# Performance work log

Measured on AMD Instinct MI355X. Metric: run time of the kernel, lower is better.

The kernel has to match this reference:

```python
import jax, jax.numpy as jnp
import numpy as np

B, Nres, TOP_K, NUM_RBF = 2, 2048, 30, 16
MAX_REL = 32  # positional clip range -> 2*32+2 = 66 classes


def _gather_nodes(nodes, idx):
    # nodes: [B, N, ...], idx: [B, N, K] -> [B, N, K, ...]
    return jax.vmap(lambda n, i: n[i])(nodes, idx)


def _rbf(D):
    # D: [..., ] -> [..., NUM_RBF]; mu in [2, 22], sigma = 20/16
    mu = jnp.linspace(2.0, 22.0, NUM_RBF)
    sigma = (22.0 - 2.0) / NUM_RBF
    return jnp.exp(-(((D[..., None] - mu) / sigma) ** 2))


def setup_inputs() -> dict:
    key = jax.random.key(0)
    ks = jax.random.split(key, 4)
    X = jax.random.normal(ks[0], (B, Nres, 4, 3), dtype=jnp.float32) * 3.0
    mask = jnp.ones((B, Nres), dtype=jnp.float32)
    residue_idx = jnp.broadcast_to(jnp.arange(Nres, dtype=jnp.int32)[None], (B, Nres))
    chain_labels = jnp.zeros((B, Nres), dtype=jnp.int32)
    w_pos = jax.random.normal(ks[1], (66, 16), dtype=jnp.float32) * 0.05
    b_pos = jax.random.normal(ks[2], (16,), dtype=jnp.float32) * 0.05
    w_edge = jax.random.normal(ks[3], (416, 128), dtype=jnp.float32) * 0.05
    ln_gamma = jnp.ones((128,), dtype=jnp.float32)
    ln_beta = jnp.zeros((128,), dtype=jnp.float32)
    return dict(X=X, mask=mask, residue_idx=residue_idx, chain_labels=chain_labels,
                w_pos=w_pos, b_pos=b_pos, w_edge=w_edge, ln_gamma=ln_gamma, ln_beta=ln_beta)


def reference(X, mask, residue_idx, chain_labels, w_pos, b_pos, w_edge, ln_gamma, ln_beta):
    # virtual C-beta from N, C, Ca (atom order in X: N=0, C=1, Ca=2, O=3)
    b = X[:, :, 2, :] - X[:, :, 0, :]
    c = X[:, :, 1, :] - X[:, :, 2, :]
    a = jnp.cross(b, c)
    Cb = -0.58273431 * a + 0.56802827 * b - 0.54067466 * c + X[:, :, 2, :]
    N_, C, Ca, O = X[:, :, 0, :], X[:, :, 1, :], X[:, :, 2, :], X[:, :, 3, :]

    # masked kNN on C atoms (ProteinFeatures._dist)
    m2 = mask[:, None, :] * mask[:, :, None]                       # [B,N,N]
    dX = C[:, None, :, :] - C[:, :, None, :]
    D = m2 * jnp.sqrt(jnp.sum(dX ** 2, -1) + 1e-6)
    D_max = jnp.max(D, -1, keepdims=True)
    D_adj = D + (1.0 - m2) * D_max
    neg, E_idx = jax.lax.top_k(-D_adj, TOP_K)                      # smallest-k
    D_neighbors = -neg                                             # [B,N,K]

    # 25-channel RBF features; gather neighbor coords instead of NxN per pair
    atoms = jnp.stack([N_, Ca, Cb, C, O], 0)                       # [5,B,N,3]
    gathered = jax.vmap(lambda A: _gather_nodes(A, E_idx))(atoms)  # [5,B,N,K,3]
    # pair order follows torch source: NN,CaCa,CbCb,CN,CCa,CCb,NCa,NCb,CbCa,
    # NC,CaC,CbC,CaN,CbN,CaCb,OO,CO,OC,NO,ON,CbO,OCa,OCb,CaO  (0=N,1=Ca,2=Cb,3=C,4=O)
    pa = jnp.array([0, 1, 2, 3, 3, 3, 0, 0, 2, 0, 1, 2, 1, 2, 1, 4, 3, 4, 0, 4, 2, 4, 4, 1])
    pb = jnp.array([0, 1, 2, 0, 1, 2, 1, 2, 1, 3, 3, 3, 0, 0, 2, 4, 4, 3, 4, 0, 4, 1, 2, 4])
    A_sel = atoms[pa]                                              # [24,B,N,3]
    Bn_sel = gathered[pb]                                          # [24,B,N,K,3]
    Dp = jnp.sqrt(jnp.sum((A_sel[:, :, :, None, :] - Bn_sel) ** 2, -1) + 1e-6)
    RBF_all = jnp.concatenate([_rbf(D_neighbors)[None], _rbf(Dp)], 0)  # [25,B,N,K,16]
    RBF_all = jnp.moveaxis(RBF_all, 0, 3).reshape(B, Nres, TOP_K, 25 * NUM_RBF)

    # positional encodings over gathered offsets / chain match
    offset = residue_idx[:, :, None] - _gather_nodes(residue_idx, E_idx)   # [B,N,K]
    E_chains = (chain_labels[:, :, None] == _gather_nodes(chain_labels, E_idx)).astype(jnp.int32)
    d = jnp.clip(offset + MAX_REL, 0, 2 * MAX_REL) * E_chains + (1 - E_chains) * (2 * MAX_REL + 1)
    E_pos = w_pos[d] + b_pos                                       # one_hot @ W == gather

    # edge embedding + layernorm
    E = jnp.concatenate([E_pos, RBF_all], -1) @ w_edge             # [B,N,K,128]
    mu = E.mean(-1, keepdims=True)
    var = E.var(-1, keepdims=True)
    E = (E - mu) / jnp.sqrt(var + 1e-5) * ln_gamma + ln_beta
    return E, E_idx
```

## Files before the change

kernel.cpp:

```cpp
#include <hip/hip_runtime.h>
#include <hip/hip_bf16.h>
#include <stdint.h>

#define BB    2
#define NRES  2048
#define TOPK  30
#define NRBF  16
#define NFEAT 416
#define NCH   128
#define NS8   108
#define NKT   13

typedef __attribute__((ext_vector_type(4))) float f32x4;
typedef unsigned long long u64;

__constant__ int c_pa[24] = {0,1,2,3,3,3,0,0,2,0,1,2,1,2,1,4,3,4,0,4,2,4,4,1};
__constant__ int c_pb[24] = {0,1,2,0,1,2,1,2,1,3,3,3,0,0,2,4,4,3,4,0,4,1,2,4};

static __device__ __forceinline__ unsigned pack4_fp8(float f0, float f1, float f2, float f3) {
  unsigned r = 0;
  r = __builtin_amdgcn_cvt_pk_fp8_f32(f0, f1, r, false);
  r = __builtin_amdgcn_cvt_pk_fp8_f32(f2, f3, r, true);
  return r;
}

__global__ __launch_bounds__(256) void prep_kernel(const float* __restrict__ X,
                                                   const float* __restrict__ w_edge,
                                                   float* __restrict__ atoms,
                                                   float4* __restrict__ Cpk,
                                                   unsigned* __restrict__ wB8) {
  if (blockIdx.x < 16) {
    int id = blockIdx.x * 256 + threadIdx.x;
    const float* x = X + (size_t)id * 12;
    float nx = x[0], ny = x[1], nz = x[2];
    float cx = x[3], cy = x[4], cz = x[5];
    float ax = x[6], ay = x[7], az = x[8];
    float ox = x[9], oy = x[10], oz = x[11];
    float bx = ax - nx, by = ay - ny, bz = az - nz;
    float ccx = cx - ax, ccy = cy - ay, ccz = cz - az;
    float crx = by * ccz - bz * ccy;
    float cry = bz * ccx - bx * ccz;
    float crz = bx * ccy - by * ccx;
    float cbx = -0.58273431f * crx + 0.56802827f * bx - 0.54067466f * ccx + ax;
    float cby = -0.58273431f * cry + 0.56802827f * by - 0.54067466f * ccy + ay;
    float cbz = -0.58273431f * crz + 0.56802827f * bz - 0.54067466f * ccz + az;
    float* r = atoms + (size_t)id * 16;
    r[0] = nx;  r[1] = ny;  r[2] = nz;
    r[3] = ax;  r[4] = ay;  r[5] = az;
    r[6] = cbx; r[7] = cby; r[8] = cbz;
    r[9] = cx;  r[10] = cy; r[11] = cz;
    r[12] = ox; r[13] = oy; r[14] = oz;
    r[15] = 0.f;
    Cpk[id] = make_float4(cx, cy, cz, 0.f);
  } else {
    int id = (blockIdx.x - 16) * 256 + threadIdx.x;
    if (id >= NFEAT * NCH / 4) return;
    int bb   = id * 4;
    int j0   = bb & 7;
    int lane = (bb >> 3) & 63;
    int nt   = (bb >> 9) & 7;
    int kt   = bb >> 12;
    int col  = nt * 16 + (lane & 15);
    int kb   = kt * 32 + ((lane >> 4) << 3) + j0;
    float f0 = w_edge[(size_t)(kb + 0) * NCH + col];
    float f1 = w_edge[(size_t)(kb + 1) * NCH + col];
    float f2 = w_edge[(size_t)(kb + 2) * NCH + col];
    float f3 = w_edge[(size_t)(kb + 3) * NCH + col];
    wB8[id] = pack4_fp8(f0, f1, f2, f3);
  }
}

__global__ __launch_bounds__(256) void topk_kernel(const float4* __restrict__ Cpk,
                                                   int* __restrict__ eidx,
                                                   float* __restrict__ dn,
                                                   float* __restrict__ outI) {
  int tid = threadIdx.x;
  int lane = tid & 63;
  int bi = blockIdx.x * 4 + (tid >> 6);
  int b = bi >> 11;
  int i = bi & (NRES - 1);
  const float4* Cb = Cpk + (size_t)b * NRES;
  float4 ci = Cb[i];

  u64 key[4][8];
  u64 sub[4];
#pragma unroll
  for (int g = 0; g < 4; ++g) {
    sub[g] = ~0ull;
#pragma unroll
    for (int s = 0; s < 8; ++s) {
      int j = lane + 64 * (g * 8 + s);
      float4 cj = Cb[j];
      float dx = cj.x - ci.x, dy = cj.y - ci.y, dz = cj.z - ci.z;
      float sm = __fadd_rn(__fadd_rn(__fadd_rn(__fmul_rn(dx, dx), __fmul_rn(dy, dy)),
                                     __fmul_rn(dz, dz)), 1e-6f);
      float d = sqrtf(sm);
      key[g][s] = ((u64)__float_as_uint(d) << 32) | (unsigned)j;
      if (key[g][s] < sub[g]) sub[g] = key[g][s];
    }
  }

  for (int k = 0; k < TOPK; ++k) {
    u64 m01 = sub[0] < sub[1] ? sub[0] : sub[1];
    u64 m23 = sub[2] < sub[3] ? sub[2] : sub[3];
    u64 gm = m01 < m23 ? m01 : m23;
#pragma unroll
    for (int off = 32; off; off >>= 1) {
      u64 o = __shfl_xor(gm, off, 64);
      if (o < gm) gm = o;
    }
    if (lane == 0) {
      int idx = (int)(unsigned)(gm & 0xffffffffu);
      eidx[(size_t)bi * TOPK + k] = idx;
      dn[(size_t)bi * TOPK + k] = __uint_as_float((unsigned)(gm >> 32));
      outI[(size_t)bi * TOPK + k] = (float)idx;
    }
#pragma unroll
    for (int g = 0; g < 4; ++g) {
      if (sub[g] == gm) {
        sub[g] = ~0ull;
#pragma unroll
        for (int s = 0; s < 8; ++s) {
          if (key[g][s] == gm) key[g][s] = ~0ull;
          if (key[g][s] < sub[g]) sub[g] = key[g][s];
        }
      }
    }
  }
}

__global__ __launch_bounds__(256) void edge_mfma_kernel(
    const float* __restrict__ atoms, const int* __restrict__ eidx_g,
    const float* __restrict__ dn_g, const int* __restrict__ ridx,
    const int* __restrict__ chain, const float* __restrict__ w_pos,
    const float* __restrict__ b_pos, const unsigned* __restrict__ wB8,
    const float* __restrict__ gamma, const float* __restrict__ beta,
    float* __restrict__ outE) {
  __shared__ __align__(16) unsigned feat8[32 * NS8];
  __shared__ float nat[TOPK][16];
  __shared__ float iat[16];
  __shared__ float dn_s[TOPK];
  __shared__ int   dsel[TOPK];
  __shared__ float2 lnp[32][4];

  int tid = threadIdx.x;
  int bi = blockIdx.x;
  int b = bi >> 11;
  int nq = tid >> 6, lane = tid & 63;
  int q = lane >> 4, ccol = lane & 15;

  if (tid < TOPK) {
    dn_s[tid] = dn_g[(size_t)bi * TOPK + tid];
    int j = eidx_g[(size_t)bi * TOPK + tid];
    int off = ridx[bi] - ridx[b * NRES + j];
    int ec = (chain[bi] == chain[b * NRES + j]) ? 1 : 0;
    int d = off + 32; d = d < 0 ? 0 : (d > 64 ? 64 : d);
    dsel[tid] = ec ? d : 65;
  }
  if (tid >= 64 && tid < 80) iat[tid - 64] = atoms[(size_t)bi * 16 + (tid - 64)];
  for (int idx = tid; idx < TOPK * 16; idx += 256) {
    int e = idx >> 4, f = idx & 15;
    nat[e][f] = atoms[((size_t)(b * NRES) + eidx_g[(size_t)bi * TOPK + e]) * 16 + f];
  }
  for (int idx = tid; idx < 2 * NS8; idx += 256)
    feat8[30 * NS8 + idx] = 0u;
  __syncthreads();

  if (tid < TOPK * 4) {
    int e = tid >> 2, p = tid & 3;
    int f0 = p * 4, ds = dsel[e];
    feat8[e * NS8 + p] = pack4_fp8(w_pos[ds * 16 + f0 + 0] + b_pos[f0 + 0],
                                   w_pos[ds * 16 + f0 + 1] + b_pos[f0 + 1],
                                   w_pos[ds * 16 + f0 + 2] + b_pos[f0 + 2],
                                   w_pos[ds * 16 + f0 + 3] + b_pos[f0 + 3]);
  }
  for (int idx = tid; idx < TOPK * 25; idx += 256) {
    int e = idx / 25, g = idx - e * 25;
    float d;
    if (g == 0) {
      d = dn_s[e];
    } else {
      int qq = g - 1;
      const float* A  = &iat[c_pa[qq] * 3];
      const float* Bv = &nat[e][c_pb[qq] * 3];
      float dx = A[0] - Bv[0], dy = A[1] - Bv[1], dz = A[2] - Bv[2];
      d = sqrtf(dx * dx + dy * dy + dz * dz + 1e-6f);
    }
    float v[16];
#pragma unroll
    for (int j = 0; j < 16; ++j) {
      float mu = 2.0f + (float)j * (20.0f / 15.0f);
      float t = (d - mu) * 0.8f;
      v[j] = __expf(-t * t);
    }
    uint4 w4 = make_uint4(pack4_fp8(v[0], v[1], v[2], v[3]),
                          pack4_fp8(v[4], v[5], v[6], v[7]),
                          pack4_fp8(v[8], v[9], v[10], v[11]),
                          pack4_fp8(v[12], v[13], v[14], v[15]));
    *(uint4*)&feat8[e * NS8 + 4 + 4 * g] = w4;
  }
  __syncthreads();

  const unsigned* ar0 = &feat8[ccol * NS8];
  const unsigned* ar1 = &feat8[(16 + ccol) * NS8];
  const u64* wBll = (const u64*)wB8;

  f32x4 acc00 = {}, acc01 = {}, acc10 = {}, acc11 = {};
#pragma unroll
  for (int kt = 0; kt < NKT; ++kt) {
    union { unsigned u[2]; long long l; } a0, a1;
    int ao = kt * 8 + q * 2;
    a0.u[0] = ar0[ao]; a0.u[1] = ar0[ao + 1];
    a1.u[0] = ar1[ao]; a1.u[1] = ar1[ao + 1];
    long long b0 = (long long)wBll[(size_t)(kt * 8 + nq * 2 + 0) * 64 + lane];
    long long b1 = (long long)wBll[(size_t)(kt * 8 + nq * 2 + 1) * 64 + lane];
    acc00 = __builtin_amdgcn_mfma_f32_16x16x32_fp8_fp8(a0.l, b0, acc00, 0, 0, 0);
    acc01 = __builtin_amdgcn_mfma_f32_16x16x32_fp8_fp8(a0.l, b1, acc01, 0, 0, 0);
    acc10 = __builtin_amdgcn_mfma_f32_16x16x32_fp8_fp8(a1.l, b0, acc10, 0, 0, 0);
    acc11 = __builtin_amdgcn_mfma_f32_16x16x32_fp8_fp8(a1.l, b1, acc11, 0, 0, 0);
  }

#pragma unroll
  for (int mh = 0; mh < 2; ++mh) {
#pragma unroll
    for (int reg = 0; reg < 4; ++reg) {
      float v0 = mh ? acc10[reg] : acc00[reg];
      float v1 = mh ? acc11[reg] : acc01[reg];
      float s = v0 + v1, ss = v0 * v0 + v1 * v1;
      s  += __shfl_xor(s, 1, 64);  ss += __shfl_xor(ss, 1, 64);
      s  += __shfl_xor(s, 2, 64);  ss += __shfl_xor(ss, 2, 64);
      s  += __shfl_xor(s, 4, 64);  ss += __shfl_xor(ss, 4, 64);
      s  += __shfl_xor(s, 8, 64);  ss += __shfl_xor(ss, 8, 64);
      if (ccol == 0) lnp[(mh << 4) + q * 4 + reg][nq] = make_float2(s, ss);
    }
  }
  __syncthreads();

  float g0 = gamma[(nq * 2 + 0) * 16 + ccol], be0 = beta[(nq * 2 + 0) * 16 + ccol];
  float g1 = gamma[(nq * 2 + 1) * 16 + ccol], be1 = beta[(nq * 2 + 1) * 16 + ccol];
#pragma unroll
  for (int mh = 0; mh < 2; ++mh) {
#pragma unroll
    for (int reg = 0; reg < 4; ++reg) {
      int m = (mh << 4) + q * 4 + reg;
      if (m < TOPK) {
        float2 p0 = lnp[m][0], p1 = lnp[m][1], p2 = lnp[m][2], p3 = lnp[m][3];
        float s = (p0.x + p1.x) + (p2.x + p3.x);
        float ss = (p0.y + p1.y) + (p2.y + p3.y);
        float mu = s * (1.0f / 128.0f);
        float var = ss * (1.0f / 128.0f) - mu * mu;
        float rstd = rsqrtf(var + 1e-5f);
        float va = mh ? acc10[reg] : acc00[reg];
        float vb = mh ? acc11[reg] : acc01[reg];
        float* o = outE + ((size_t)bi * TOPK + m) * NCH + ccol;
        o[(nq * 2 + 0) * 16] = (va - mu) * rstd * g0 + be0;
        o[(nq * 2 + 1) * 16] = (vb - mu) * rstd * g1 + be1;
      }
    }
  }
}

extern "C" void kernel_launch(void* const* d_in, const int* in_sizes, int n_in,
                              void* d_out, int out_size, void* d_ws, size_t ws_size,
                              hipStream_t stream) {
  const float* X      = (const float*)d_in[0];
  const int*   ridx   = (const int*)d_in[2];
  const int*   chain  = (const int*)d_in[3];
  const float* w_pos  = (const float*)d_in[4];
  const float* b_pos  = (const float*)d_in[5];
  const float* w_edge = (const float*)d_in[6];
  const float* gamma  = (const float*)d_in[7];
  const float* beta   = (const float*)d_in[8];

  float* outE = (float*)d_out;
  float* outI = outE + (size_t)BB * NRES * TOPK * NCH;

  char* p = (char*)d_ws;
  float* atoms = (float*)p;                 p += (size_t)BB * NRES * 16 * 4;
  int*   eidx  = (int*)p;                   p += (size_t)BB * NRES * TOPK * 4;
  float* dn    = (float*)p;                 p += (size_t)BB * NRES * TOPK * 4;
  unsigned* wB8 = (unsigned*)p;             p += (size_t)NCH * NFEAT;
  float4* Cpk  = (float4*)p;

  prep_kernel<<<16 + (NFEAT * NCH / 4 + 255) / 256, 256, 0, stream>>>(X, w_edge, atoms, Cpk, wB8);
  topk_kernel<<<BB * NRES / 4, 256, 0, stream>>>(Cpk, eidx, dn, outI);
  edge_mfma_kernel<<<BB * NRES, 256, 0, stream>>>(atoms, eidx, dn, ridx, chain,
                                                  w_pos, b_pos, wB8, gamma, beta, outE);
}
```

Measured before the change: 77.38 us.

## Extract two minima per top-k round and process two residues per edge block

The top-k kernel now tracks the two smallest keys per group and merges top-2 pairs across the wavefront, so each round emits two neighbors. This halves the number of shuffle-reduction rounds at the cost of more compare work per round. The edge MFMA kernel now handles two residues per block, reusing each loaded weight fragment across twice as many MFMAs and halving the block count. The price is more LDS per block and more accumulator registers, which may lower occupancy.

New measurement: 93.81 us. 1.21x slower.

```diff
diff --git a/kernel.cpp b/kernel.cpp
--- a/kernel.cpp
+++ b/kernel.cpp
@@ -10,6 +10,7 @@
 #define NCH   128
 #define NS8   108
 #define NKT   13
+#define RPB   2
 
 typedef __attribute__((ext_vector_type(4))) float f32x4;
 typedef unsigned long long u64;
@@ -23,6 +24,8 @@
   r = __builtin_amdgcn_cvt_pk_fp8_f32(f2, f3, r, true);
   return r;
 }
+static __device__ __forceinline__ u64 umin64(u64 a, u64 b) { return a < b ? a : b; }
+static __device__ __forceinline__ u64 umax64(u64 a, u64 b) { return a > b ? a : b; }
 
 __global__ __launch_bounds__(256) void prep_kernel(const float* __restrict__ X,
                                                    const float* __restrict__ w_edge,
@@ -62,11 +65,10 @@
     int kt   = bb >> 12;
     int col  = nt * 16 + (lane & 15);
     int kb   = kt * 32 + ((lane >> 4) << 3) + j0;
-    float f0 = w_edge[(size_t)(kb + 0) * NCH + col];
-    float f1 = w_edge[(size_t)(kb + 1) * NCH + col];
-    float f2 = w_edge[(size_t)(kb + 2) * NCH + col];
-    float f3 = w_edge[(size_t)(kb + 3) * NCH + col];
-    wB8[id] = pack4_fp8(f0, f1, f2, f3);
+    wB8[id] = pack4_fp8(w_edge[(size_t)(kb + 0) * NCH + col],
+                        w_edge[(size_t)(kb + 1) * NCH + col],
+                        w_edge[(size_t)(kb + 2) * NCH + col],
+                        w_edge[(size_t)(kb + 3) * NCH + col]);
   }
 }
 
@@ -83,10 +85,10 @@
   float4 ci = Cb[i];
 
   u64 key[4][8];
-  u64 sub[4];
+  u64 g1[4], g2[4];
 #pragma unroll
   for (int g = 0; g < 4; ++g) {
-    sub[g] = ~0ull;
+    g1[g] = ~0ull; g2[g] = ~0ull;
 #pragma unroll
     for (int s = 0; s < 8; ++s) {
       int j = lane + 64 * (g * 8 + s);
@@ -95,35 +97,49 @@
       float sm = __fadd_rn(__fadd_rn(__fadd_rn(__fmul_rn(dx, dx), __fmul_rn(dy, dy)),
                                      __fmul_rn(dz, dz)), 1e-6f);
       float d = sqrtf(sm);
-      key[g][s] = ((u64)__float_as_uint(d) << 32) | (unsigned)j;
-      if (key[g][s] < sub[g]) sub[g] = key[g][s];
-    }
-  }
-
-  for (int k = 0; k < TOPK; ++k) {
-    u64 m01 = sub[0] < sub[1] ? sub[0] : sub[1];
-    u64 m23 = sub[2] < sub[3] ? sub[2] : sub[3];
-    u64 gm = m01 < m23 ? m01 : m23;
+      u64 kk = ((u64)__float_as_uint(d) << 32) | (unsigned)j;
+      key[g][s] = kk;
+      if (kk < g1[g]) { g2[g] = g1[g]; g1[g] = kk; }
+      else if (kk < g2[g]) g2[g] = kk;
+    }
+  }
+
+  for (int kk2 = 0; kk2 < TOPK / 2; ++kk2) {
+    u64 x1 = umin64(g1[0], g1[1]);
+    u64 x2 = umin64(umax64(g1[0], g1[1]), umin64(g2[0], g2[1]));
+    u64 y1 = umin64(g1[2], g1[3]);
+    u64 y2 = umin64(umax64(g1[2], g1[3]), umin64(g2[2], g2[3]));
+    u64 m1 = umin64(x1, y1);
+    u64 m2 = umin64(umax64(x1, y1), umin64(x2, y2));
 #pragma unroll
     for (int off = 32; off; off >>= 1) {
-      u64 o = __shfl_xor(gm, off, 64);
-      if (o < gm) gm = o;
+      u64 o1 = __shfl_xor(m1, off, 64);
+      u64 o2 = __shfl_xor(m2, off, 64);
+      u64 n1 = umin64(m1, o1);
+      u64 n2 = umin64(umax64(m1, o1), umin64(m2, o2));
+      m1 = n1; m2 = n2;
     }
     if (lane == 0) {
-      int idx = (int)(unsigned)(gm & 0xffffffffu);
-      eidx[(size_t)bi * TOPK + k] = idx;
-      dn[(size_t)bi * TOPK + k] = __uint_as_float((unsigned)(gm >> 32));
-      outI[(size_t)bi * TOPK + k] = (float)idx;
+      int i1 = (int)(unsigned)m1, i2 = (int)(unsigned)m2;
+      size_t o = (size_t)bi * TOPK + 2 * kk2;
+      eidx[o] = i1;           eidx[o + 1] = i2;
+      dn[o]   = __uint_as_float((unsigned)(m1 >> 32));
+      dn[o+1] = __uint_as_float((unsigned)(m2 >> 32));
+      outI[o] = (float)i1;    outI[o + 1] = (float)i2;
     }
 #pragma unroll
     for (int g = 0; g < 4; ++g) {
-      if (sub[g] == gm) {
-        sub[g] = ~0ull;
+      bool hit = (g1[g] == m1) | (g1[g] == m2) | (g2[g] == m2);
+      if (hit) {
+        u64 n1 = ~0ull, n2 = ~0ull;
 #pragma unroll
         for (int s = 0; s < 8; ++s) {
-          if (key[g][s] == gm) key[g][s] = ~0ull;
-          if (key[g][s] < sub[g]) sub[g] = key[g][s];
+          u64 kv = key[g][s];
+          if (kv == m1 || kv == m2) { kv = ~0ull; key[g][s] = kv; }
+          if (kv < n1) { n2 = n1; n1 = kv; }
+          else if (kv < n2) n2 = kv;
         }
+        g1[g] = n1; g2[g] = n2;
       }
     }
   }
@@ -136,52 +152,62 @@
     const float* __restrict__ b_pos, const unsigned* __restrict__ wB8,
     const float* __restrict__ gamma, const float* __restrict__ beta,
     float* __restrict__ outE) {
-  __shared__ __align__(16) unsigned feat8[32 * NS8];
-  __shared__ float nat[TOPK][16];
-  __shared__ float iat[16];
-  __shared__ float dn_s[TOPK];
-  __shared__ int   dsel[TOPK];
-  __shared__ float2 lnp[32][4];
+  __shared__ __align__(16) unsigned feat8[RPB * 32 * NS8];
+  __shared__ float nat[RPB * TOPK][16];
+  __shared__ float iat[RPB][16];
+  __shared__ float dn_s[RPB * TOPK];
+  __shared__ int   dsel[RPB * TOPK];
+  __shared__ float2 lnp[RPB][32][4];
 
   int tid = threadIdx.x;
-  int bi = blockIdx.x;
-  int b = bi >> 11;
+  int bi0 = blockIdx.x * RPB;
+  int b = bi0 >> 11;
   int nq = tid >> 6, lane = tid & 63;
   int q = lane >> 4, ccol = lane & 15;
 
-  if (tid < TOPK) {
-    dn_s[tid] = dn_g[(size_t)bi * TOPK + tid];
-    int j = eidx_g[(size_t)bi * TOPK + tid];
-    int off = ridx[bi] - ridx[b * NRES + j];
-    int ec = (chain[bi] == chain[b * NRES + j]) ? 1 : 0;
+  if (tid < RPB * TOPK) {
+    int gi = bi0 + tid / TOPK;
+    int k = tid % TOPK;
+    dn_s[tid] = dn_g[(size_t)gi * TOPK + k];
+    int j = eidx_g[(size_t)gi * TOPK + k];
+    int off = ridx[gi] - ridx[b * NRES + j];
+    int ec = (chain[gi] == chain[b * NRES + j]) ? 1 : 0;
     int d = off + 32; d = d < 0 ? 0 : (d > 64 ? 64 : d);
     dsel[tid] = ec ? d : 65;
   }
-  if (tid >= 64 && tid < 80) iat[tid - 64] = atoms[(size_t)bi * 16 + (tid - 64)];
-  for (int idx = tid; idx < TOPK * 16; idx += 256) {
+  if (tid >= 64 && tid < 64 + RPB * 16) {
+    int t = tid - 64;
+    iat[t >> 4][t & 15] = atoms[((size_t)bi0 + (t >> 4)) * 16 + (t & 15)];
+  }
+  for (int idx = tid; idx < RPB * TOPK * 16; idx += 256) {
     int e = idx >> 4, f = idx & 15;
-    nat[e][f] = atoms[((size_t)(b * NRES) + eidx_g[(size_t)bi * TOPK + e]) * 16 + f];
-  }
-  for (int idx = tid; idx < 2 * NS8; idx += 256)
-    feat8[30 * NS8 + idx] = 0u;
+    int gi = bi0 + e / TOPK;
+    nat[e][f] = atoms[((size_t)(b * NRES) + eidx_g[(size_t)gi * TOPK + (e % TOPK)]) * 16 + f];
+  }
+  for (int idx = tid; idx < RPB * 2 * NS8; idx += 256) {
+    int r = idx / (2 * NS8), rem = idx % (2 * NS8);
+    feat8[(r * 32 + 30) * NS8 + rem] = 0u;
+  }
   __syncthreads();
 
-  if (tid < TOPK * 4) {
+  if (tid < RPB * TOPK * 4) {
     int e = tid >> 2, p = tid & 3;
     int f0 = p * 4, ds = dsel[e];
-    feat8[e * NS8 + p] = pack4_fp8(w_pos[ds * 16 + f0 + 0] + b_pos[f0 + 0],
-                                   w_pos[ds * 16 + f0 + 1] + b_pos[f0 + 1],
-                                   w_pos[ds * 16 + f0 + 2] + b_pos[f0 + 2],
-                                   w_pos[ds * 16 + f0 + 3] + b_pos[f0 + 3]);
-  }
-  for (int idx = tid; idx < TOPK * 25; idx += 256) {
+    int r = e / TOPK, k = e % TOPK;
+    feat8[(r * 32 + k) * NS8 + p] = pack4_fp8(w_pos[ds * 16 + f0 + 0] + b_pos[f0 + 0],
+                                              w_pos[ds * 16 + f0 + 1] + b_pos[f0 + 1],
+                                              w_pos[ds * 16 + f0 + 2] + b_pos[f0 + 2],
+                                              w_pos[ds * 16 + f0 + 3] + b_pos[f0 + 3]);
+  }
+  for (int idx = tid; idx < RPB * TOPK * 25; idx += 256) {
     int e = idx / 25, g = idx - e * 25;
+    int r = e / TOPK, k = e - r * TOPK;
     float d;
     if (g == 0) {
       d = dn_s[e];
     } else {
       int qq = g - 1;
-      const float* A  = &iat[c_pa[qq] * 3];
+      const float* A  = &iat[r][c_pa[qq] * 3];
       const float* Bv = &nat[e][c_pb[qq] * 3];
       float dx = A[0] - Bv[0], dy = A[1] - Bv[1], dz = A[2] - Bv[2];
       d = sqrtf(dx * dx + dy * dy + dz * dz + 1e-6f);
@@ -197,41 +223,54 @@
                           pack4_fp8(v[4], v[5], v[6], v[7]),
                           pack4_fp8(v[8], v[9], v[10], v[11]),
                           pack4_fp8(v[12], v[13], v[14], v[15]));
-    *(uint4*)&feat8[e * NS8 + 4 + 4 * g] = w4;
+    *(uint4*)&feat8[(r * 32 + k) * NS8 + 4 + 4 * g] = w4;
   }
   __syncthreads();
 
-  const unsigned* ar0 = &feat8[ccol * NS8];
-  const unsigned* ar1 = &feat8[(16 + ccol) * NS8];
+  const unsigned* ar00 = &feat8[(0 * 32 + ccol) * NS8];
+  const unsigned* ar01 = &feat8[(0 * 32 + 16 + ccol) * NS8];
+  const unsigned* ar10 = &feat8[(1 * 32 + ccol) * NS8];
+  const unsigned* ar11 = &feat8[(1 * 32 + 16 + ccol) * NS8];
   const u64* wBll = (const u64*)wB8;
 
-  f32x4 acc00 = {}, acc01 = {}, acc10 = {}, acc11 = {};
+  f32x4 a000 = {}, a001 = {}, a010 = {}, a011 = {};
+  f32x4 a100 = {}, a101 = {}, a110 = {}, a111 = {};
 #pragma unroll
   for (int kt = 0; kt < NKT; ++kt) {
-    union { unsigned u[2]; long long l; } a0, a1;
+    union { unsigned u[2]; long long l; } f00, f01, f10, f11;
     int ao = kt * 8 + q * 2;
-    a0.u[0] = ar0[ao]; a0.u[1] = ar0[ao + 1];
-    a1.u[0] = ar1[ao]; a1.u[1] = ar1[ao + 1];
+    f00.u[0] = ar00[ao]; f00.u[1] = ar00[ao + 1];
+    f01.u[0] = ar01[ao]; f01.u[1] = ar01[ao + 1];
+    f10.u[0] = ar10[ao]; f10.u[1] = ar10[ao + 1];
+    f11.u[0] = ar11[ao]; f11.u[1] = ar11[ao + 1];
     long long b0 = (long long)wBll[(size_t)(kt * 8 + nq * 2 + 0) * 64 + lane];
     long long b1 = (long long)wBll[(size_t)(kt * 8 + nq * 2 + 1) * 64 + lane];
-    acc00 = __builtin_amdgcn_mfma_f32_16x16x32_fp8_fp8(a0.l, b0, acc00, 0, 0, 0);
-    acc01 = __builtin_amdgcn_mfma_f32_16x16x32_fp8_fp8(a0.l, b1, acc01, 0, 0, 0);
-    acc10 = __builtin_amdgcn_mfma_f32_16x16x32_fp8_fp8(a1.l, b0, acc10, 0, 0, 0);
-    acc11 = __builtin_amdgcn_mfma_f32_16x16x32_fp8_fp8(a1.l, b1, acc11, 0, 0, 0);
-  }
-
-#pragma unroll
-  for (int mh = 0; mh < 2; ++mh) {
-#pragma unroll
-    for (int reg = 0; reg < 4; ++reg) {
-      float v0 = mh ? acc10[reg] : acc00[reg];
-      float v1 = mh ? acc11[reg] : acc01[reg];
-      float s = v0 + v1, ss = v0 * v0 + v1 * v1;
-      s  += __shfl_xor(s, 1, 64);  ss += __shfl_xor(ss, 1, 64);
-      s  += __shfl_xor(s, 2, 64);  ss += __shfl_xor(ss, 2, 64);
-      s  += __shfl_xor(s, 4, 64);  ss += __shfl_xor(ss, 4, 64);
-      s  += __shfl_xor(s, 8, 64);  ss += __shfl_xor(ss, 8, 64);
-      if (ccol == 0) lnp[(mh << 4) + q * 4 + reg][nq] = make_float2(s, ss);
+    a000 = __builtin_amdgcn_mfma_f32_16x16x32_fp8_fp8(f00.l, b0, a000, 0, 0, 0);
+    a001 = __builtin_amdgcn_mfma_f32_16x16x32_fp8_fp8(f00.l, b1, a001, 0, 0, 0);
+    a010 = __builtin_amdgcn_mfma_f32_16x16x32_fp8_fp8(f01.l, b0, a010, 0, 0, 0);
+    a011 = __builtin_amdgcn_mfma_f32_16x16x32_fp8_fp8(f01.l, b1, a011, 0, 0, 0);
+    a100 = __builtin_amdgcn_mfma_f32_16x16x32_fp8_fp8(f10.l, b0, a100, 0, 0, 0);
+    a101 = __builtin_amdgcn_mfma_f32_16x16x32_fp8_fp8(f10.l, b1, a101, 0, 0, 0);
+    a110 = __builtin_amdgcn_mfma_f32_16x16x32_fp8_fp8(f11.l, b0, a110, 0, 0, 0);
+    a111 = __builtin_amdgcn_mfma_f32_16x16x32_fp8_fp8(f11.l, b1, a111, 0, 0, 0);
+  }
+
+#pragma unroll
+  for (int r = 0; r < RPB; ++r) {
+#pragma unroll
+    for (int mh = 0; mh < 2; ++mh) {
+#pragma unroll
+      for (int reg = 0; reg < 4; ++reg) {
+        float v0, v1;
+        if (r == 0) { v0 = mh ? a010[reg] : a000[reg]; v1 = mh ? a011[reg] : a001[reg]; }
+        else        { v0 = mh ? a110[reg] : a100[reg]; v1 = mh ? a111[reg] : a101[reg]; }
+        float s = v0 + v1, ss = v0 * v0 + v1 * v1;
+        s  += __shfl_xor(s, 1, 64);  ss += __shfl_xor(ss, 1, 64);
+        s  += __shfl_xor(s, 2, 64);  ss += __shfl_xor(ss, 2, 64);
+        s  += __shfl_xor(s, 4, 64);  ss += __shfl_xor(ss, 4, 64);
+        s  += __shfl_xor(s, 8, 64);  ss += __shfl_xor(ss, 8, 64);
+        if (ccol == 0) lnp[r][(mh << 4) + q * 4 + reg][nq] = make_float2(s, ss);
+      }
     }
   }
   __syncthreads();
@@ -239,22 +278,26 @@
   float g0 = gamma[(nq * 2 + 0) * 16 + ccol], be0 = beta[(nq * 2 + 0) * 16 + ccol];
   float g1 = gamma[(nq * 2 + 1) * 16 + ccol], be1 = beta[(nq * 2 + 1) * 16 + ccol];
 #pragma unroll
-  for (int mh = 0; mh < 2; ++mh) {
-#pragma unroll
-    for (int reg = 0; reg < 4; ++reg) {
-      int m = (mh << 4) + q * 4 + reg;
-      if (m < TOPK) {
-        float2 p0 = lnp[m][0], p1 = lnp[m][1], p2 = lnp[m][2], p3 = lnp[m][3];
-        float s = (p0.x + p1.x) + (p2.x + p3.x);
-        float ss = (p0.y + p1.y) + (p2.y + p3.y);
-        float mu = s * (1.0f / 128.0f);
-        float var = ss * (1.0f / 128.0f) - mu * mu;
-        float rstd = rsqrtf(var + 1e-5f);
-        float va = mh ? acc10[reg] : acc00[reg];
-        float vb = mh ? acc11[reg] : acc01[reg];
-        float* o = outE + ((size_t)bi * TOPK + m) * NCH + ccol;
-        o[(nq * 2 + 0) * 16] = (va - mu) * rstd * g0 + be0;
-        o[(nq * 2 + 1) * 16] = (vb - mu) * rstd * g1 + be1;
+  for (int r = 0; r < RPB; ++r) {
+#pragma unroll
+    for (int mh = 0; mh < 2; ++mh) {
+#pragma unroll
+      for (int reg = 0; reg < 4; ++reg) {
+        int m = (mh << 4) + q * 4 + reg;
+        if (m < TOPK) {
+          float2 p0 = lnp[r][m][0], p1 = lnp[r][m][1], p2 = lnp[r][m][2], p3 = lnp[r][m][3];
+          float s = (p0.x + p1.x) + (p2.x + p3.x);
+          float ss = (p0.y + p1.y) + (p2.y + p3.y);
+          float mu = s * (1.0f / 128.0f);
+          float var = ss * (1.0f / 128.0f) - mu * mu;
+          float rstd = rsqrtf(var + 1e-5f);
+          float va, vb;
+          if (r == 0) { va = mh ? a010[reg] : a000[reg]; vb = mh ? a011[reg] : a001[reg]; }
+          else        { va = mh ? a110[reg] : a100[reg]; vb = mh ? a111[reg] : a101[reg]; }
+          float* o = outE + ((size_t)(bi0 + r) * TOPK + m) * NCH + ccol;
+          o[(nq * 2 + 0) * 16] = (va - mu) * rstd * g0 + be0;
+          o[(nq * 2 + 1) * 16] = (vb - mu) * rstd * g1 + be1;
+        }
       }
     }
   }
@@ -284,6 +327,6 @@
 
   prep_kernel<<<16 + (NFEAT * NCH / 4 + 255) / 256, 256, 0, stream>>>(X, w_edge, atoms, Cpk, wB8);
   topk_kernel<<<BB * NRES / 4, 256, 0, stream>>>(Cpk, eidx, dn, outI);
-  edge_mfma_kernel<<<BB * NRES, 256, 0, stream>>>(atoms, eidx, dn, ridx, chain,
-                                                  w_pos, b_pos, wB8, gamma, beta, outE);
-}
+  edge_mfma_kernel<<<BB * NRES / RPB, 256, 0, stream>>>(atoms, eidx, dn, ridx, chain,
+                                                        w_pos, b_pos, wB8, gamma, beta, outE);
+}
```
